# Kernel optimization log

Hardware: AMD Instinct MI355X
Metric: run time of the kernel (lower is better)

Reference implementation:

```python
import jax, jax.numpy as jnp
import numpy as np

B, DIM, H, W = 16, 256, 64, 64
HEADS, DHEAD, MEM = 4, 32, 4
HIDDEN = HEADS * DHEAD


def setup_inputs() -> dict:
    key = jax.random.key(0)
    ks = jax.random.split(key, 4)
    return {
        "x": jax.random.normal(ks[0], (B, DIM, H, W), dtype=jnp.float32),
        "g1": jnp.ones((DIM,), dtype=jnp.float32),
        "w_qkv": jax.random.normal(ks[1], (3 * HIDDEN, DIM), dtype=jnp.float32) * 0.02,
        "mem_kv": jax.random.normal(ks[2], (2, HEADS, DHEAD, MEM), dtype=jnp.float32),
        "w_out": jax.random.normal(ks[3], (DIM, HIDDEN), dtype=jnp.float32) * 0.02,
        "b_out": jnp.zeros((DIM,), dtype=jnp.float32),
        "g2": jnp.ones((DIM,), dtype=jnp.float32),
    }


def _rmsnorm(x, g):
    # F.normalize(x, dim=1) * g * sqrt(dim); g broadcast over (1, dim, 1, 1)
    n = jnp.sqrt(jnp.sum(x * x, axis=1, keepdims=True))
    scale = jnp.asarray(x.shape[1], x.dtype) ** 0.5
    return x / jnp.maximum(n, 1e-12) * g[None, :, None, None] * scale


def reference(x, g1, w_qkv, mem_kv, w_out, b_out, g2):
    b, c, h, w = x.shape
    attn_scale = DHEAD ** -0.5
    xn = _rmsnorm(x, g1)
    # 1x1 conv == channel matmul; chunk(3, dim=1) -> leading axis 3 after reshape
    qkv = jnp.einsum('oc,bchw->bohw', w_qkv, xn)
    qkv = qkv.reshape(b, 3, HEADS, DHEAD, h * w)  # b 3 h d n
    q, k, v = qkv[:, 0], qkv[:, 1], qkv[:, 2]
    mk = jnp.broadcast_to(mem_kv[0][None], (b, HEADS, DHEAD, MEM))
    mv = jnp.broadcast_to(mem_kv[1][None], (b, HEADS, DHEAD, MEM))
    k = jnp.concatenate([mk, k], axis=-1)  # b h d (m+n)
    v = jnp.concatenate([mv, v], axis=-1)
    q = jax.nn.softmax(q, axis=-2) * attn_scale  # softmax over feature dim d
    k = jax.nn.softmax(k, axis=-1)               # softmax over token dim n
    context = jnp.einsum('bhdn,bhen->bhde', k, v)  # d x e per head
    out = jnp.einsum('bhde,bhdn->bhen', context, q)
    out = out.reshape(b, HIDDEN, h, w)
    out = jnp.einsum('oc,bchw->bohw', w_out, out) + b_out[None, :, None, None]
    return _rmsnorm(out, g2)
```

## Files before the change

kernel.cpp:

```cpp
#include <hip/hip_runtime.h>
#include <hip/hip_bf16.h>

#define NB 16
#define DIM 256
#define HW 4096
#define HEADS 4
#define DHEAD 32
#define MEM 4
#define HIDDEN 128

typedef __hip_bfloat16 bf16;
typedef __attribute__((ext_vector_type(8))) short bf16x8;
typedef __attribute__((ext_vector_type(4))) float f32x4;
typedef __attribute__((ext_vector_type(4))) unsigned short us4;

#define AS1 __attribute__((address_space(1)))
#define AS3 __attribute__((address_space(3)))

__device__ __forceinline__ void gld_lds16(const void* g, void* l) {
    __builtin_amdgcn_global_load_lds((const AS1 void*)g, (AS3 void*)l, 16, 0, 0);
}
__device__ __forceinline__ float b2f(short s) {
    union { unsigned int u; float f; } x; x.u = ((unsigned int)(unsigned short)s) << 16; return x.f;
}
__device__ __forceinline__ short f2bs(float f) {
    bf16 h = __float2bfloat16(f);
    return *reinterpret_cast<short*>(&h);
}

constexpr size_t OFF_W1B  = 0;
constexpr size_t OFF_RP   = OFF_W1B + 98304*2;
constexpr size_t OFF_PCTX = OFF_RP + 4*65536*4;
constexpr size_t OFF_CTXN = OFF_PCTX + (size_t)32*64*1056*4;
constexpr size_t OFF_M    = OFF_CTXN + (size_t)64*1024*4;
constexpr size_t OFF_QT   = OFF_M + (size_t)NB*DIM*HIDDEN*2;
constexpr size_t OFF_XT   = OFF_QT + (size_t)NB*HW*HIDDEN*2;

__global__ void k_prep(const float* __restrict__ wqkv, const float* __restrict__ g1,
                       short* __restrict__ w1b) {
    int i = blockIdx.x * 256 + threadIdx.x;
    w1b[i] = f2bs(wqkv[i] * g1[i & (DIM - 1)]);
}

__global__ __launch_bounds__(256) void k_tr(const float* __restrict__ x,
                                            short* __restrict__ xT,
                                            float* __restrict__ rpart) {
    int n0 = blockIdx.x * 64, cy = blockIdx.y, b = blockIdx.z;
    int c0 = cy * 64;
    __shared__ short xs[64 * 65];
    __shared__ float ps[4][64];
    int t = threadIdx.x;
    int ln = t & 63, cb = t >> 6;
    const float* xp = x + ((size_t)b * DIM + c0) * HW + n0;
    float ss = 0.f;
#pragma unroll
    for (int j = 0; j < 16; ++j) {
        int c = cb * 16 + j;
        float v = xp[(size_t)c * HW + ln];
        ss += v * v;
        xs[c * 65 + ln] = f2bs(v);
    }
    ps[cb][ln] = ss;
    __syncthreads();
    if (t < 64)
        rpart[((size_t)cy * NB + b) * HW + n0 + t] = ps[0][t] + ps[1][t] + ps[2][t] + ps[3][t];
    int n = t >> 2, ch = t & 3;
    alignas(16) short tmp[16];
#pragma unroll
    for (int i = 0; i < 16; ++i) tmp[i] = xs[(ch * 16 + i) * 65 + n];
    short* o = xT + ((size_t)b * HW + n0 + n) * DIM + c0 + ch * 16;
    *(bf16x8*)(o)     = *(bf16x8*)(tmp);
    *(bf16x8*)(o + 8) = *(bf16x8*)(tmp + 8);
}

__global__ __launch_bounds__(768, 1) void k_gemm(const short* __restrict__ w1b,
                                                 const short* __restrict__ xT,
                                                 const float* __restrict__ rpart,
                                                 short* __restrict__ qT,
                                                 float* __restrict__ pctx) {
    extern __shared__ __align__(16) char smem[];
    int nt = blockIdx.x, b = blockIdx.y;
    int t = threadIdx.x;
    int w = t >> 6, lane = t & 63;
    int wr = w >> 1, wc = w & 1;
    int lr = lane & 15, lg = lane >> 4;
    const f32x4 fz = {0.f, 0.f, 0.f, 0.f};
    f32x4 acc[4][4];
#pragma unroll
    for (int m = 0; m < 4; ++m)
#pragma unroll
        for (int n = 0; n < 4; ++n) acc[m][n] = fz;

    const short* Bg = xT + ((size_t)b * HW + nt * 128) * 256;

    auto STAGE = [&](int kt, int buf) {
        int kk = kt * 64;
        char* asb = smem + buf * 49152;
        char* bsb = smem + 98304 + buf * 16384;
#pragma unroll
        for (int is = 0; is < 4; ++is) {
            int o = is * 12288 + t * 16;
            int row = o >> 7;
            int js = ((o >> 4) & 7) ^ (row & 7);
            gld_lds16(w1b + (size_t)row * 256 + kk + js * 8, asb + o);
        }
        {
            int o = t * 16;
            int row = o >> 7;
            int js = ((o >> 4) & 7) ^ (row & 7);
            gld_lds16(Bg + (size_t)row * 256 + kk + js * 8, bsb + o);
        }
        if (t < 256) {
            int o = 12288 + t * 16;
            int row = o >> 7;
            int js = ((o >> 4) & 7) ^ (row & 7);
            gld_lds16(Bg + (size_t)row * 256 + kk + js * 8, bsb + o);
        }
    };

    STAGE(0, 0);
    asm volatile("s_waitcnt vmcnt(0)" ::: "memory");
    __builtin_amdgcn_s_barrier();

#pragma unroll
    for (int kt = 0; kt < 4; ++kt) {
        int buf = kt & 1;
        if (kt < 3) STAGE(kt + 1, buf ^ 1);
        const char* asb = smem + buf * 49152;
        const char* bsb = smem + 98304 + buf * 16384;
        __builtin_amdgcn_s_setprio(1);
#pragma unroll
        for (int ks = 0; ks < 2; ++ks) {
            int j = lg + 4 * ks;
            bf16x8 av[4], bv[4];
#pragma unroll
            for (int m = 0; m < 4; ++m) {
                int row = wr * 64 + m * 16 + lr;
                av[m] = *(const bf16x8*)(asb + row * 128 + ((j ^ (row & 7)) << 4));
            }
#pragma unroll
            for (int nf = 0; nf < 4; ++nf) {
                int row = wc * 64 + nf * 16 + lr;
                bv[nf] = *(const bf16x8*)(bsb + row * 128 + ((j ^ (row & 7)) << 4));
            }
#pragma unroll
            for (int m = 0; m < 4; ++m)
#pragma unroll
                for (int nf = 0; nf < 4; ++nf)
                    acc[m][nf] = __builtin_amdgcn_mfma_f32_16x16x32_bf16(av[m], bv[nf], acc[m][nf], 0, 0, 0);
        }
        __builtin_amdgcn_s_setprio(0);
        asm volatile("s_waitcnt vmcnt(0)" ::: "memory");
        __builtin_amdgcn_s_barrier();
    }

    int gcol0 = nt * 128 + wc * 64 + lr;
    float rv[4];
#pragma unroll
    for (int nf = 0; nf < 4; ++nf) {
        int col = gcol0 + nf * 16;
        float s = rpart[(size_t)b * HW + col] + rpart[(size_t)(16 + b) * HW + col]
                + rpart[(size_t)(32 + b) * HW + col] + rpart[(size_t)(48 + b) * HW + col];
        rv[nf] = 16.0f / fmaxf(sqrtf(s), 1e-12f);
    }

    short* ekb = (short*)smem;
    short* vb  = (short*)(smem + 32768);

    if (wr < 2) {
#pragma unroll
        for (int nf = 0; nf < 4; ++nf) {
            int gcol = gcol0 + nf * 16;
#pragma unroll
            for (int a = 0; a < 2; ++a) {
                float v[8];
#pragma unroll
                for (int mm = 0; mm < 2; ++mm)
#pragma unroll
                    for (int q = 0; q < 4; ++q)
                        v[mm * 4 + q] = acc[2 * a + mm][nf][q] * rv[nf];
                float mx = v[0];
#pragma unroll
                for (int i = 1; i < 8; ++i) mx = fmaxf(mx, v[i]);
                mx = fmaxf(mx, __shfl_xor(mx, 16));
                mx = fmaxf(mx, __shfl_xor(mx, 32));
                float sum = 0.f;
#pragma unroll
                for (int i = 0; i < 8; ++i) { v[i] = __expf(v[i] - mx); sum += v[i]; }
                sum += __shfl_xor(sum, 16);
                sum += __shfl_xor(sum, 32);
                float inv = 0.17677669529663689f / sum;
                size_t base = ((size_t)b * HW + gcol) * 128 + (wr * 2 + a) * 32 + lg * 4;
#pragma unroll
                for (int mm = 0; mm < 2; ++mm) {
                    us4 pk;
#pragma unroll
                    for (int q = 0; q < 4; ++q)
                        pk[q] = (unsigned short)f2bs(v[mm * 4 + q] * inv);
                    *(us4*)(qT + base + mm * 16) = pk;
                }
            }
        }
    } else if (wr < 4) {
#pragma unroll
        for (int m = 0; m < 4; ++m)
#pragma unroll
            for (int nf = 0; nf < 4; ++nf)
#pragma unroll
                for (int q = 0; q < 4; ++q) {
                    int rloc = (wr - 2) * 64 + m * 16 + lg * 4 + q;
                    int col = wc * 64 + nf * 16 + lr;
                    int cs = ((((col >> 3) ^ (rloc & 15)) << 3) | (col & 7));
                    ekb[rloc * 128 + cs] = f2bs(__expf(acc[m][nf][q] * rv[nf]));
                }
    } else {
#pragma unroll
        for (int m = 0; m < 4; ++m)
#pragma unroll
            for (int nf = 0; nf < 4; ++nf)
#pragma unroll
                for (int q = 0; q < 4; ++q) {
                    int rloc = (wr - 4) * 64 + m * 16 + lg * 4 + q;
                    int col = wc * 64 + nf * 16 + lr;
                    int cs = ((((col >> 3) ^ (rloc & 15)) << 3) | (col & 7));
                    vb[rloc * 128 + cs] = f2bs(acc[m][nf][q] * rv[nf]);
                }
    }
    __syncthreads();
    if (w < 4) {
        int h = w;
        f32x4 c2[2][2];
        c2[0][0] = fz; c2[0][1] = fz; c2[1][0] = fz; c2[1][1] = fz;
#pragma unroll
        for (int ks = 0; ks < 4; ++ks) {
            int j = ks * 4 + lg;
            bf16x8 a2[2], b2[2];
#pragma unroll
            for (int mm = 0; mm < 2; ++mm) {
                int row = h * 32 + mm * 16 + lr;
                a2[mm] = *(const bf16x8*)(ekb + row * 128 + ((j ^ (row & 15)) << 3));
            }
#pragma unroll
            for (int nn = 0; nn < 2; ++nn) {
                int row = h * 32 + nn * 16 + lr;
                b2[nn] = *(const bf16x8*)(vb + row * 128 + ((j ^ (row & 15)) << 3));
            }
#pragma unroll
            for (int mm = 0; mm < 2; ++mm)
#pragma unroll
                for (int nn = 0; nn < 2; ++nn)
                    c2[mm][nn] = __builtin_amdgcn_mfma_f32_16x16x32_bf16(a2[mm], b2[nn], c2[mm][nn], 0, 0, 0);
        }
        float* o = pctx + ((size_t)nt * 64 + b * 4 + h) * 1056;
#pragma unroll
        for (int mm = 0; mm < 2; ++mm)
#pragma unroll
            for (int nn = 0; nn < 2; ++nn)
#pragma unroll
                for (int qq = 0; qq < 4; ++qq) {
                    int d = mm * 16 + lg * 4 + qq;
                    int e = nn * 16 + lr;
                    o[d * 32 + e] = c2[mm][nn][qq];
                }
    } else if (w >= 8) {
        int hd = (w - 8) * 32 + (lane & 31);
        int half = lane >> 5;
        float rs = 0.f;
#pragma unroll
        for (int blk = 0; blk < 8; ++blk) {
            int chunk = half * 8 + blk;
            bf16x8 e8 = *(const bf16x8*)(ekb + hd * 128 + ((chunk ^ (hd & 15)) << 3));
#pragma unroll
            for (int jj = 0; jj < 8; ++jj) rs += b2f(e8[jj]);
        }
        rs += __shfl_xor(rs, 32);
        if (lane < 32)
            pctx[((size_t)nt * 64 + b * 4 + (w - 8)) * 1056 + 1024 + (lane & 31)] = rs;
    }
}

__global__ __launch_bounds__(256) void k_red(const float* __restrict__ pctx,
                                             const float* __restrict__ memkv,
                                             float* __restrict__ ctxn) {
    int ds = blockIdx.x, bh = blockIdx.y;
    int t = threadIdx.x;
    int dd = t >> 5, ee = t & 31;
    int d = ds * 8 + dd;
    int h = bh & 3;
    __shared__ float rss[8];
    float s = 0.f;
#pragma unroll 8
    for (int c = 0; c < 32; ++c)
        s += pctx[((size_t)c * 64 + bh) * 1056 + d * 32 + ee];
    if (t < 8) {
        int d2 = ds * 8 + t;
        float rs = 0.f;
#pragma unroll 8
        for (int c = 0; c < 32; ++c)
            rs += pctx[((size_t)c * 64 + bh) * 1056 + 1024 + d2];
#pragma unroll
        for (int m2 = 0; m2 < MEM; ++m2) rs += __expf(memkv[(h * 32 + d2) * MEM + m2]);
        rss[t] = rs;
    }
    float mem = 0.f;
#pragma unroll
    for (int m2 = 0; m2 < MEM; ++m2)
        mem += __expf(memkv[(h * 32 + d) * MEM + m2]) * memkv[512 + (h * 32 + ee) * MEM + m2];
    __syncthreads();
    ctxn[(size_t)bh * 1024 + d * 32 + ee] = (s + mem) / rss[dd];
}

__global__ __launch_bounds__(256) void k_M2(const float* __restrict__ ctxn,
                                            const float* __restrict__ wout,
                                            short* __restrict__ Mmat) {
    int og = blockIdx.x, b = blockIdx.y;
    __shared__ float ctx[4 * 33 * 33];
    __shared__ float wsw[32 * 136];
    int t = threadIdx.x;
#pragma unroll
    for (int j = 0; j < 16; ++j) {
        int e = t + j * 256;
        int h = e >> 10, dd = (e >> 5) & 31, ee = e & 31;
        ctx[h * 1089 + dd * 33 + ee] = ctxn[(size_t)(b * 4 + h) * 1024 + (e & 1023)];
    }
#pragma unroll
    for (int j = 0; j < 4; ++j) {
        int e4 = t + j * 256;
        int row = e4 >> 5, c = (e4 & 31) * 4;
        f32x4 w4 = *(const f32x4*)(wout + (size_t)(og * 32 + row) * HIDDEN + c);
        *(f32x4*)(wsw + row * 136 + (c >> 5) * 34 + (c & 31)) = w4;
    }
    __syncthreads();
    int ol = t >> 3, hg = t & 7;
    alignas(16) short out16[16];
#pragma unroll
    for (int ii = 0; ii < 16; ++ii) {
        int hd = hg * 16 + ii;
        int h = hd >> 5, dd = hd & 31;
        float s = 0.f;
#pragma unroll
        for (int e = 0; e < 32; ++e)
            s += wsw[ol * 136 + h * 34 + e] * ctx[h * 1089 + dd * 33 + e];
        out16[ii] = f2bs(s);
    }
    short* op = Mmat + ((size_t)(b * 256 + og * 32 + ol)) * 128 + hg * 16;
    *(bf16x8*)(op)     = *(bf16x8*)(out16);
    *(bf16x8*)(op + 8) = *(bf16x8*)(out16 + 8);
}

__global__ __launch_bounds__(256) void k_out2(const short* __restrict__ Mmat,
                                              const short* __restrict__ qT,
                                              const float* __restrict__ bout,
                                              const float* __restrict__ g2,
                                              float* __restrict__ out) {
    int nt = blockIdx.x, b = blockIdx.y;
    __shared__ short As[256 * 64];
    __shared__ short Bs[64 * 64];
    __shared__ float sw[4][80];
    __shared__ float r2s[64];
    int t = threadIdx.x;
    int wave = t >> 6, lane = t & 63;
    int lr = lane & 15, lg = lane >> 4;
    const short* Ag = Mmat + (size_t)b * 256 * 128;
    const short* Bg = qT + ((size_t)b * HW + nt * 64) * 128;
    const f32x4 fz = {0.f, 0.f, 0.f, 0.f};
    f32x4 acc[4][4];
#pragma unroll
    for (int m = 0; m < 4; ++m)
#pragma unroll
        for (int n = 0; n < 4; ++n) acc[m][n] = fz;

    for (int kk = 0; kk < 128; kk += 64) {
        if (kk) __syncthreads();
#pragma unroll
        for (int is = 0; is < 8; ++is) {
            int o = is * 4096 + t * 16;
            int rr2 = o >> 7;
            int js = ((o >> 4) & 7) ^ (rr2 & 7);
            gld_lds16(Ag + (size_t)rr2 * 128 + kk + js * 8, (char*)As + o);
        }
#pragma unroll
        for (int is = 0; is < 2; ++is) {
            int o = is * 4096 + t * 16;
            int rr2 = o >> 7;
            int js = ((o >> 4) & 7) ^ (rr2 & 7);
            gld_lds16(Bg + (size_t)rr2 * 128 + kk + js * 8, (char*)Bs + o);
        }
        __syncthreads();
#pragma unroll
        for (int ks = 0; ks < 2; ++ks) {
            bf16x8 av[4], bv[4];
            int j = lg + 4 * ks;
#pragma unroll
            for (int m = 0; m < 4; ++m) {
                int row = wave * 64 + m * 16 + lr;
                av[m] = *(const bf16x8*)((const char*)As + row * 128 + ((j ^ (row & 7)) << 4));
            }
#pragma unroll
            for (int n = 0; n < 4; ++n) {
                int row = n * 16 + lr;
                bv[n] = *(const bf16x8*)((const char*)Bs + row * 128 + ((j ^ (row & 7)) << 4));
            }
#pragma unroll
            for (int m = 0; m < 4; ++m)
#pragma unroll
                for (int n = 0; n < 4; ++n)
                    acc[m][n] = __builtin_amdgcn_mfma_f32_16x16x32_bf16(av[m], bv[n], acc[m][n], 0, 0, 0);
        }
    }
    float bb[4][4], gg[4][4];
#pragma unroll
    for (int m = 0; m < 4; ++m)
#pragma unroll
        for (int q = 0; q < 4; ++q) {
            int row = wave * 64 + m * 16 + lg * 4 + q;
            bb[m][q] = bout[row];
            gg[m][q] = g2[row];
        }
    float ssn[4] = {0.f, 0.f, 0.f, 0.f};
#pragma unroll
    for (int n = 0; n < 4; ++n)
#pragma unroll
        for (int m = 0; m < 4; ++m)
#pragma unroll
            for (int q = 0; q < 4; ++q) {
                float val = acc[m][n][q] + bb[m][q];
                acc[m][n][q] = val;
                ssn[n] += val * val;
            }
#pragma unroll
    for (int n = 0; n < 4; ++n) {
        ssn[n] += __shfl_xor(ssn[n], 16);
        ssn[n] += __shfl_xor(ssn[n], 32);
    }
    if (lg == 0) {
#pragma unroll
        for (int n = 0; n < 4; ++n) sw[wave][n * 16 + lr] = ssn[n];
    }
    __syncthreads();
    if (t < 64) {
        float s = sw[0][t] + sw[1][t] + sw[2][t] + sw[3][t];
        r2s[t] = 16.0f / fmaxf(sqrtf(s), 1e-12f);
    }
    __syncthreads();
    float* op = out + (size_t)b * DIM * HW + nt * 64;
#pragma unroll
    for (int n = 0; n < 4; ++n) {
        float rc = r2s[n * 16 + lr];
#pragma unroll
        for (int m = 0; m < 4; ++m)
#pragma unroll
            for (int q = 0; q < 4; ++q) {
                int row = wave * 64 + m * 16 + lg * 4 + q;
                op[(size_t)row * HW + n * 16 + lr] = acc[m][n][q] * rc * gg[m][q];
            }
    }
}

extern "C" void kernel_launch(void* const* d_in, const int* in_sizes, int n_in,
                              void* d_out, int out_size, void* d_ws, size_t ws_size,
                              hipStream_t stream) {
    const float* x     = (const float*)d_in[0];
    const float* g1    = (const float*)d_in[1];
    const float* wqkv  = (const float*)d_in[2];
    const float* memkv = (const float*)d_in[3];
    const float* wout  = (const float*)d_in[4];
    const float* bout  = (const float*)d_in[5];
    const float* g2    = (const float*)d_in[6];
    float* out = (float*)d_out;
    char* ws = (char*)d_ws;

    short* w1b  = (short*)(ws + OFF_W1B);
    float* rpart= (float*)(ws + OFF_RP);
    float* pctx = (float*)(ws + OFF_PCTX);
    float* ctxn = (float*)(ws + OFF_CTXN);
    short* Mmat = (short*)(ws + OFF_M);
    short* qT   = (short*)(ws + OFF_QT);
    short* xT   = (short*)(ws + OFF_XT);

    hipFuncSetAttribute((const void*)k_gemm,
                        hipFuncAttributeMaxDynamicSharedMemorySize, 131072);

    k_prep<<<384, 256, 0, stream>>>(wqkv, g1, w1b);
    k_tr<<<dim3(64, 4, NB), 256, 0, stream>>>(x, xT, rpart);
    k_gemm<<<dim3(32, NB), 768, 131072, stream>>>(w1b, xT, rpart, qT, pctx);
    k_red<<<dim3(4, 64), 256, 0, stream>>>(pctx, memkv, ctxn);
    k_M2<<<dim3(8, NB), 256, 0, stream>>>(ctxn, wout, Mmat);
    k_out2<<<dim3(64, NB), 256, 0, stream>>>(Mmat, qT, bout, g2, out);
}
```

Measured before the change: 78.09 us.

## Fold weight prep into transpose kernel and halve GEMM K-tile to shrink LDS

Removes the separate k_prep launch by having the first 384 blocks of k_tr also scale and convert w_qkv to bf16. Separately, k_gemm's K-step shrinks from 64 to 32 (8 iterations instead of 4), which cuts double-buffered LDS from 128KB dynamic to 64KB static and drops the occupancy-1 launch bound. The goal is one less launch and possibly two blocks per CU. The cost is more barriers and waits per K-loop, and the epilogue's shared-memory reuse (offset 32768 onward) must fit in the smaller buffer.

```diff
diff --git a/kernel.cpp b/kernel.cpp
--- a/kernel.cpp
+++ b/kernel.cpp
@@ -36,20 +36,22 @@
 constexpr size_t OFF_QT   = OFF_M + (size_t)NB*DIM*HIDDEN*2;
 constexpr size_t OFF_XT   = OFF_QT + (size_t)NB*HW*HIDDEN*2;
 
-__global__ void k_prep(const float* __restrict__ wqkv, const float* __restrict__ g1,
-                       short* __restrict__ w1b) {
-    int i = blockIdx.x * 256 + threadIdx.x;
-    w1b[i] = f2bs(wqkv[i] * g1[i & (DIM - 1)]);
-}
-
 __global__ __launch_bounds__(256) void k_tr(const float* __restrict__ x,
+                                            const float* __restrict__ wqkv,
+                                            const float* __restrict__ g1,
                                             short* __restrict__ xT,
-                                            float* __restrict__ rpart) {
+                                            float* __restrict__ rpart,
+                                            short* __restrict__ w1b) {
+    int t = threadIdx.x;
+    int fid = blockIdx.x + (blockIdx.y << 6) + (blockIdx.z << 8);
+    if (fid < 384) {
+        int i = fid * 256 + t;
+        w1b[i] = f2bs(wqkv[i] * g1[i & (DIM - 1)]);
+    }
     int n0 = blockIdx.x * 64, cy = blockIdx.y, b = blockIdx.z;
     int c0 = cy * 64;
     __shared__ short xs[64 * 65];
     __shared__ float ps[4][64];
-    int t = threadIdx.x;
     int ln = t & 63, cb = t >> 6;
     const float* xp = x + ((size_t)b * DIM + c0) * HW + n0;
     float ss = 0.f;
@@ -73,12 +75,12 @@
     *(bf16x8*)(o + 8) = *(bf16x8*)(tmp + 8);
 }
 
-__global__ __launch_bounds__(768, 1) void k_gemm(const short* __restrict__ w1b,
-                                                 const short* __restrict__ xT,
-                                                 const float* __restrict__ rpart,
-                                                 short* __restrict__ qT,
-                                                 float* __restrict__ pctx) {
-    extern __shared__ __align__(16) char smem[];
+__global__ __launch_bounds__(768) void k_gemm(const short* __restrict__ w1b,
+                                              const short* __restrict__ xT,
+                                              const float* __restrict__ rpart,
+                                              short* __restrict__ qT,
+                                              float* __restrict__ pctx) {
+    __shared__ __align__(16) char smem[65536];
     int nt = blockIdx.x, b = blockIdx.y;
     int t = threadIdx.x;
     int w = t >> 6, lane = t & 63;
@@ -94,26 +96,20 @@
     const short* Bg = xT + ((size_t)b * HW + nt * 128) * 256;
 
     auto STAGE = [&](int kt, int buf) {
-        int kk = kt * 64;
-        char* asb = smem + buf * 49152;
-        char* bsb = smem + 98304 + buf * 16384;
-#pragma unroll
-        for (int is = 0; is < 4; ++is) {
+        int kk = kt * 32;
+        char* asb = smem + buf * 24576;
+        char* bsb = smem + 49152 + buf * 8192;
+#pragma unroll
+        for (int is = 0; is < 2; ++is) {
             int o = is * 12288 + t * 16;
-            int row = o >> 7;
-            int js = ((o >> 4) & 7) ^ (row & 7);
+            int row = o >> 6;
+            int js = ((o >> 4) & 3) ^ (row & 3);
             gld_lds16(w1b + (size_t)row * 256 + kk + js * 8, asb + o);
         }
-        {
+        if (t < 512) {
             int o = t * 16;
-            int row = o >> 7;
-            int js = ((o >> 4) & 7) ^ (row & 7);
-            gld_lds16(Bg + (size_t)row * 256 + kk + js * 8, bsb + o);
-        }
-        if (t < 256) {
-            int o = 12288 + t * 16;
-            int row = o >> 7;
-            int js = ((o >> 4) & 7) ^ (row & 7);
+            int row = o >> 6;
+            int js = ((o >> 4) & 3) ^ (row & 3);
             gld_lds16(Bg + (size_t)row * 256 + kk + js * 8, bsb + o);
         }
     };
@@ -123,32 +119,28 @@
     __builtin_amdgcn_s_barrier();
 
 #pragma unroll
-    for (int kt = 0; kt < 4; ++kt) {
+    for (int kt = 0; kt < 8; ++kt) {
         int buf = kt & 1;
-        if (kt < 3) STAGE(kt + 1, buf ^ 1);
-        const char* asb = smem + buf * 49152;
-        const char* bsb = smem + 98304 + buf * 16384;
+        if (kt < 7) STAGE(kt + 1, buf ^ 1);
+        const char* asb = smem + buf * 24576;
+        const char* bsb = smem + 49152 + buf * 8192;
+        bf16x8 av[4], bv[4];
         __builtin_amdgcn_s_setprio(1);
 #pragma unroll
-        for (int ks = 0; ks < 2; ++ks) {
-            int j = lg + 4 * ks;
-            bf16x8 av[4], bv[4];
-#pragma unroll
-            for (int m = 0; m < 4; ++m) {
-                int row = wr * 64 + m * 16 + lr;
-                av[m] = *(const bf16x8*)(asb + row * 128 + ((j ^ (row & 7)) << 4));
-            }
-#pragma unroll
-            for (int nf = 0; nf < 4; ++nf) {
-                int row = wc * 64 + nf * 16 + lr;
-                bv[nf] = *(const bf16x8*)(bsb + row * 128 + ((j ^ (row & 7)) << 4));
-            }
-#pragma unroll
-            for (int m = 0; m < 4; ++m)
-#pragma unroll
-                for (int nf = 0; nf < 4; ++nf)
-                    acc[m][nf] = __builtin_amdgcn_mfma_f32_16x16x32_bf16(av[m], bv[nf], acc[m][nf], 0, 0, 0);
-        }
+        for (int m = 0; m < 4; ++m) {
+            int row = wr * 64 + m * 16 + lr;
+            av[m] = *(const bf16x8*)(asb + row * 64 + ((lg ^ (row & 3)) << 4));
+        }
+#pragma unroll
+        for (int nf = 0; nf < 4; ++nf) {
+            int row = wc * 64 + nf * 16 + lr;
+            bv[nf] = *(const bf16x8*)(bsb + row * 64 + ((lg ^ (row & 3)) << 4));
+        }
+#pragma unroll
+        for (int m = 0; m < 4; ++m)
+#pragma unroll
+            for (int nf = 0; nf < 4; ++nf)
+                acc[m][nf] = __builtin_amdgcn_mfma_f32_16x16x32_bf16(av[m], bv[nf], acc[m][nf], 0, 0, 0);
         __builtin_amdgcn_s_setprio(0);
         asm volatile("s_waitcnt vmcnt(0)" ::: "memory");
         __builtin_amdgcn_s_barrier();
@@ -478,12 +470,8 @@
     short* qT   = (short*)(ws + OFF_QT);
     short* xT   = (short*)(ws + OFF_XT);
 
-    hipFuncSetAttribute((const void*)k_gemm,
-                        hipFuncAttributeMaxDynamicSharedMemorySize, 131072);
-
-    k_prep<<<384, 256, 0, stream>>>(wqkv, g1, w1b);
-    k_tr<<<dim3(64, 4, NB), 256, 0, stream>>>(x, xT, rpart);
-    k_gemm<<<dim3(32, NB), 768, 131072, stream>>>(w1b, xT, rpart, qT, pctx);
+    k_tr<<<dim3(64, 4, NB), 256, 0, stream>>>(x, wqkv, g1, xT, rpart, w1b);
+    k_gemm<<<dim3(32, NB), 768, 0, stream>>>(w1b, xT, rpart, qT, pctx);
     k_red<<<dim3(4, 64), 256, 0, stream>>>(pctx, memkv, ctxn);
     k_M2<<<dim3(8, NB), 256, 0, stream>>>(ctxn, wout, Mmat);
     k_out2<<<dim3(64, NB), 256, 0, stream>>>(Mmat, qT, bout, g2, out);
```

New measurement: 75.45 us. -3.4%, faster.
